# Kernel tuning notes

Hardware: AMD Instinct MI355X
Metric: run time of the kernel (lower is better)

Reference implementation:

```python
import jax, jax.numpy as jnp
import numpy as np

LN_EPS = 1e-5
L2_EPS = 1e-6
TAU = 0.07

def _proj(x, W, b, g, be):
    # Linear + LayerNorm (dropout is identity in eval)
    y = x @ W.T + b
    mu = jnp.mean(y, axis=-1, keepdims=True)
    var = jnp.var(y, axis=-1, keepdims=True)
    return (y - mu) * jax.lax.rsqrt(var + LN_EPS) * g + be

def _l2norm(x):
    return x / (jnp.linalg.norm(x, axis=-1, keepdims=True) + L2_EPS)

def setup_inputs() -> dict:
    key = jax.random.key(0)
    ks = iter(jax.random.split(key, 16))
    B, C, D = 2048, 512, 256
    dims = {"text": 1024, "image": 1024, "audio": 512, "tab": 256}
    inp = {}
    for n, d in dims.items():
        inp[f"f_{n}"] = jax.random.normal(next(ks), (B, d), jnp.float32)
        inp[f"W_{n}"] = jax.random.normal(next(ks), (D, d), jnp.float32) * (1.0 / np.sqrt(d))
        inp[f"b_{n}"] = jnp.zeros((D,), jnp.float32)
        inp[f"g_{n}"] = jnp.ones((D,), jnp.float32)
        inp[f"be_{n}"] = jnp.zeros((D,), jnp.float32)
    inp["U"] = jax.random.normal(next(ks), (C, D), jnp.float32) * (1.0 / np.sqrt(D))
    inp["O"] = jax.random.normal(next(ks), (C, D), jnp.float32) * (1.0 / np.sqrt(D))
    inp["cls_bias"] = jnp.zeros((C,), jnp.float32)
    return inp

def reference(f_text, f_image, f_audio, f_tab,
              W_text, b_text, g_text, be_text,
              W_image, b_image, g_image, be_image,
              W_audio, b_audio, g_audio, be_audio,
              W_tab, b_tab, g_tab, be_tab,
              U, O, cls_bias):
    # Per-modality projection -> Z: [B, M, D]
    Z = jnp.stack([
        _proj(f_text, W_text, b_text, g_text, be_text),
        _proj(f_image, W_image, b_image, g_image, be_image),
        _proj(f_audio, W_audio, b_audio, g_audio, be_audio),
        _proj(f_tab, W_tab, b_tab, g_tab, be_tab),
    ], axis=1)
    Zn = _l2norm(Z)            # [B, M, D]
    Un = _l2norm(U)            # [C, D]
    sim = jnp.einsum('bmd,cd->bmc', Zn, Un) / max(TAU, 1e-6)
    r = jax.nn.softmax(sim, axis=1)                 # softmax over modalities M
    Cmix = jnp.einsum('bmc,bmd->bcd', r, Z)         # [B, C, D]
    logits = jnp.einsum('cd,bcd->bc', O, Cmix) + cls_bias
    OjZi = jnp.einsum('cd,bmd->bmc', O, Z)
    contrib = OjZi * r
    return logits, r, sim, contrib
```

## Files before the change

### kernel.cpp

```cpp
#include <hip/hip_runtime.h>
#include <math.h>

typedef __attribute__((ext_vector_type(8))) short short8;
typedef __attribute__((ext_vector_type(4))) float f32x4;

constexpr int Bn = 2048, Mn = 4, Cn = 512, Dn = 256;
constexpr size_t LOGITS_OFF = 0;
constexpr size_t R_OFF   = (size_t)Bn * Cn;
constexpr size_t SIM_OFF = R_OFF + (size_t)Bn * Mn * Cn;
constexpr size_t CTR_OFF = SIM_OFF + (size_t)Bn * Mn * Cn;
constexpr float INV_TAU = 1.0f / 0.07f;

__device__ __forceinline__ unsigned short f2bf(float f) {
  unsigned u = __float_as_uint(f);
  u += 0x7fffu + ((u >> 16) & 1u);
  return (unsigned short)(u >> 16);
}

__device__ __forceinline__ void gload16(const void* g, void* l) {
  __builtin_amdgcn_global_load_lds(
      (const __attribute__((address_space(1))) void*)g,
      (__attribute__((address_space(3))) void*)l, 16, 0, 0);
}

struct CvtArgs {
  const float* src[6];
  unsigned short* dst[6];
  int n[6];
};

__global__ __launch_bounds__(256) void cvt_kernel(CvtArgs a) {
  int arr = blockIdx.y;
  int idx = (blockIdx.x * 256 + threadIdx.x) * 8;
  if (idx >= a.n[arr]) return;
  const float4* s = (const float4*)(a.src[arr] + idx);
  float4 v0 = s[0], v1 = s[1];
  uint4 p;
  p.x = f2bf(v0.x) | ((unsigned)f2bf(v0.y) << 16);
  p.y = f2bf(v0.z) | ((unsigned)f2bf(v0.w) << 16);
  p.z = f2bf(v1.x) | ((unsigned)f2bf(v1.y) << 16);
  p.w = f2bf(v1.z) | ((unsigned)f2bf(v1.w) << 16);
  *(uint4*)(a.dst[arr] + idx) = p;
}

__global__ __launch_bounds__(256) void invu_kernel(const float* __restrict__ U,
                                                   float* __restrict__ invU) {
  int c = blockIdx.x * 4 + (threadIdx.x >> 6);
  int lane = threadIdx.x & 63;
  float4 v = *(const float4*)&U[(size_t)c * Dn + lane * 4];
  float s = v.x*v.x + v.y*v.y + v.z*v.z + v.w*v.w;
  #pragma unroll
  for (int m = 32; m >= 1; m >>= 1) s += __shfl_xor(s, m, 64);
  if (lane == 0) invU[c] = 1.0f / (sqrtf(s) + 1e-6f);
}

struct ProjArgs {
  const float* f[4];
  const float* b[4];
  const float* g[4];
  const float* be[4];
  const unsigned short* Wb[4];
  int K[4];
};

__global__ __launch_bounds__(128) void proj_kernel(ProjArgs a,
                                                   unsigned short* __restrict__ Zb,
                                                   float* __restrict__ invZ) {
  const int m = blockIdx.y;
  const int row0 = blockIdx.x * 32;
  const int K = a.K[m];
  const float* __restrict__ F = a.f[m];
  const unsigned short* __restrict__ Wm = a.Wb[m];

  __shared__ unsigned short aS[4 * 32 * 8];
  __shared__ unsigned short bS[4 * 256 * 8];
  __shared__ unsigned short zS[32][264];

  const int tid = threadIdx.x;
  const int w = tid >> 6;
  const int l = tid & 63;
  const int rg = l >> 4, c16 = l & 15;

  f32x4 acc[16];
  #pragma unroll
  for (int i = 0; i < 16; i++) acc[i] = (f32x4){0.f, 0.f, 0.f, 0.f};

  const int abase = ((l >> 4) * 32 + w * 16 + c16) * 8;
  const int bbase = ((l >> 4) * 256 + c16) * 8;

  const int akc = tid >> 5;
  const int arow = tid & 31;
  const float* fsrc = F + (size_t)(row0 + arow) * K + akc * 8;

  for (int k0 = 0; k0 < K; k0 += 32) {
    #pragma unroll
    for (int ii = 0; ii < 8; ii++) {
      int i = w + 2 * ii;
      int kc = i >> 2, col = (i & 3) * 64 + l;
      gload16(Wm + (size_t)col * K + k0 + kc * 8, &bS[i * 512]);
    }
    {
      const float4* s = (const float4*)(fsrc + k0);
      float4 v0 = s[0], v1 = s[1];
      uint4 p;
      p.x = f2bf(v0.x) | ((unsigned)f2bf(v0.y) << 16);
      p.y = f2bf(v0.z) | ((unsigned)f2bf(v0.w) << 16);
      p.z = f2bf(v1.x) | ((unsigned)f2bf(v1.y) << 16);
      p.w = f2bf(v1.z) | ((unsigned)f2bf(v1.w) << 16);
      *(uint4*)&aS[tid * 8] = p;
    }
    __syncthreads();
    short8 av = *(const short8*)&aS[abase];
    #pragma unroll
    for (int nf = 0; nf < 16; nf++) {
      short8 bv = *(const short8*)&bS[bbase + nf * 128];
      acc[nf] = __builtin_amdgcn_mfma_f32_16x16x32_bf16(av, bv, acc[nf], 0, 0, 0);
    }
    __syncthreads();
  }

  float bb[16], gg[16], ee[16];
  #pragma unroll
  for (int nf = 0; nf < 16; nf++) {
    bb[nf] = a.b[m][nf * 16 + c16];
    gg[nf] = a.g[m][nf * 16 + c16];
    ee[nf] = a.be[m][nf * 16 + c16];
  }
  float s[4] = {0, 0, 0, 0}, s2[4] = {0, 0, 0, 0};
  #pragma unroll
  for (int nf = 0; nf < 16; nf++) {
    #pragma unroll
    for (int j = 0; j < 4; j++) {
      float y = acc[nf][j] + bb[nf];
      acc[nf][j] = y;
      s[j] += y; s2[j] += y * y;
    }
  }
  #pragma unroll
  for (int msk = 8; msk >= 1; msk >>= 1) {
    #pragma unroll
    for (int j = 0; j < 4; j++) {
      s[j]  += __shfl_xor(s[j],  msk, 64);
      s2[j] += __shfl_xor(s2[j], msk, 64);
    }
  }
  float mu[4], rs[4];
  #pragma unroll
  for (int j = 0; j < 4; j++) {
    mu[j] = s[j] * (1.0f / 256.0f);
    float var = s2[j] * (1.0f / 256.0f) - mu[j] * mu[j];
    rs[j] = rsqrtf(var + 1e-5f);
  }
  float zs[4] = {0, 0, 0, 0};
  #pragma unroll
  for (int nf = 0; nf < 16; nf++) {
    #pragma unroll
    for (int j = 0; j < 4; j++) {
      float z = (acc[nf][j] - mu[j]) * rs[j] * gg[nf] + ee[nf];
      acc[nf][j] = z;
      zs[j] += z * z;
    }
  }
  #pragma unroll
  for (int msk = 8; msk >= 1; msk >>= 1) {
    #pragma unroll
    for (int j = 0; j < 4; j++) zs[j] += __shfl_xor(zs[j], msk, 64);
  }
  float inv[4];
  #pragma unroll
  for (int j = 0; j < 4; j++) inv[j] = 1.0f / (sqrtf(zs[j]) + 1e-6f);

  if (c16 < 4) {
    float v = (c16 == 0) ? inv[0] : (c16 == 1) ? inv[1] : (c16 == 2) ? inv[2] : inv[3];
    int local = w * 16 + rg * 4 + c16;
    invZ[(size_t)(row0 + local) * 4 + m] = v;
  }
  #pragma unroll
  for (int nf = 0; nf < 16; nf++) {
    #pragma unroll
    for (int j = 0; j < 4; j++)
      zS[w * 16 + rg * 4 + j][nf * 16 + c16] = f2bf(acc[nf][j]);
  }
  __syncthreads();
  #pragma unroll
  for (int i = 0; i < 8; i++) {
    int c = tid + i * 128;
    int row = c >> 5, colc = (c & 31) * 8;
    uint4 v = *(const uint4*)&zS[row][colc];
    *(uint4*)(Zb + ((size_t)(row0 + row) * 4 + m) * 256 + colc) = v;
  }
}

__global__ __launch_bounds__(256) void dual_kernel(
    const unsigned short* __restrict__ Zb,
    const unsigned short* __restrict__ Ub,
    const unsigned short* __restrict__ Ob,
    const float* __restrict__ invZ, const float* __restrict__ invU,
    const float* __restrict__ cls_bias, float* __restrict__ out) {
  const int row0 = blockIdx.x * 64;
  const int col0 = blockIdx.y * 128;

  __shared__ unsigned short aS[4 * 64 * 8];
  __shared__ unsigned short uS[4 * 128 * 8];
  __shared__ unsigned short oS[4 * 128 * 8];

  const int tid = threadIdx.x;
  const int w = tid >> 6, l = tid & 63;
  const int wm = w >> 1, wc = w & 1;
  const int rg = l >> 4, c16 = l & 15;

  f32x4 accU[2][4], accO[2][4];
  #pragma unroll
  for (int i = 0; i < 2; i++)
    #pragma unroll
    for (int j = 0; j < 4; j++) {
      accU[i][j] = (f32x4){0.f, 0.f, 0.f, 0.f};
      accO[i][j] = (f32x4){0.f, 0.f, 0.f, 0.f};
    }

  const int abase = ((l >> 4) * 64 + wm * 32 + c16) * 8;
  const int ubase = ((l >> 4) * 128 + wc * 64 + c16) * 8;

  for (int k0 = 0; k0 < 256; k0 += 32) {
    #pragma unroll
    for (int ii = 0; ii < 5; ii++) {
      int i = w + 4 * ii;
      if (i < 4) {
        gload16(Zb + (size_t)(row0 + l) * 256 + k0 + i * 8, &aS[i * 512]);
      } else if (i < 12) {
        int j = i - 4;
        int kc = j >> 1, col = (j & 1) * 64 + l;
        gload16(Ub + (size_t)(col0 + col) * 256 + k0 + kc * 8, &uS[j * 512]);
      } else {
        int j = i - 12;
        int kc = j >> 1, col = (j & 1) * 64 + l;
        gload16(Ob + (size_t)(col0 + col) * 256 + k0 + kc * 8, &oS[j * 512]);
      }
    }
    __syncthreads();
    short8 av0 = *(const short8*)&aS[abase];
    short8 av1 = *(const short8*)&aS[abase + 128];
    #pragma unroll
    for (int nf = 0; nf < 4; nf++) {
      short8 uv = *(const short8*)&uS[ubase + nf * 128];
      accU[0][nf] = __builtin_amdgcn_mfma_f32_16x16x32_bf16(av0, uv, accU[0][nf], 0, 0, 0);
      accU[1][nf] = __builtin_amdgcn_mfma_f32_16x16x32_bf16(av1, uv, accU[1][nf], 0, 0, 0);
      short8 ov = *(const short8*)&oS[ubase + nf * 128];
      accO[0][nf] = __builtin_amdgcn_mfma_f32_16x16x32_bf16(av0, ov, accO[0][nf], 0, 0, 0);
      accO[1][nf] = __builtin_amdgcn_mfma_f32_16x16x32_bf16(av1, ov, accO[1][nf], 0, 0, 0);
    }
    __syncthreads();
  }

  #pragma unroll
  for (int mf = 0; mf < 2; mf++) {
    int bmb = row0 + wm * 32 + mf * 16 + rg * 4;
    f32x4 iz = *(const f32x4*)&invZ[bmb];
    int bidx = bmb >> 2;
    #pragma unroll
    for (int nf = 0; nf < 4; nf++) {
      int col = col0 + wc * 64 + nf * 16 + c16;
      float iu = invU[col] * INV_TAU;
      f32x4 sU = accU[mf][nf], sO = accO[mf][nf];
      float sim0 = sU[0] * iz[0] * iu;
      float sim1 = sU[1] * iz[1] * iu;
      float sim2 = sU[2] * iz[2] * iu;
      float sim3 = sU[3] * iz[3] * iu;
      float mx = fmaxf(fmaxf(sim0, sim1), fmaxf(sim2, sim3));
      float e0 = __expf(sim0 - mx), e1 = __expf(sim1 - mx);
      float e2 = __expf(sim2 - mx), e3 = __expf(sim3 - mx);
      float rinv = 1.0f / (e0 + e1 + e2 + e3);
      float r0 = e0 * rinv, r1 = e1 * rinv, r2 = e2 * rinv, r3 = e3 * rinv;
      float ct0 = sO[0] * r0, ct1 = sO[1] * r1, ct2 = sO[2] * r2, ct3 = sO[3] * r3;
      size_t sb = (size_t)bmb * Cn + col;
      out[SIM_OFF + sb]          = sim0;
      out[SIM_OFF + sb + Cn]     = sim1;
      out[SIM_OFF + sb + 2*Cn]   = sim2;
      out[SIM_OFF + sb + 3*Cn]   = sim3;
      out[R_OFF + sb]            = r0;
      out[R_OFF + sb + Cn]       = r1;
      out[R_OFF + sb + 2*Cn]     = r2;
      out[R_OFF + sb + 3*Cn]     = r3;
      out[CTR_OFF + sb]          = ct0;
      out[CTR_OFF + sb + Cn]     = ct1;
      out[CTR_OFF + sb + 2*Cn]   = ct2;
      out[CTR_OFF + sb + 3*Cn]   = ct3;
      out[LOGITS_OFF + (size_t)bidx * Cn + col] =
          ct0 + ct1 + ct2 + ct3 + cls_bias[col];
    }
  }
}

extern "C" void kernel_launch(void* const* d_in, const int* in_sizes, int n_in,
                              void* d_out, int out_size, void* d_ws, size_t ws_size,
                              hipStream_t stream) {
  const int fi[4] = {0, 5, 10, 15};
  const int Ks[4] = {1024, 1024, 512, 256};

  char* ws = (char*)d_ws;
  unsigned short* Zb  = (unsigned short*)(ws + 0);
  unsigned short* Wb0 = (unsigned short*)(ws + 4194304);
  unsigned short* Wb1 = (unsigned short*)(ws + 4718592);
  unsigned short* Wb2 = (unsigned short*)(ws + 5242880);
  unsigned short* Wb3 = (unsigned short*)(ws + 5505024);
  unsigned short* Ub  = (unsigned short*)(ws + 5636096);
  unsigned short* Ob  = (unsigned short*)(ws + 5898240);
  float* invZ         = (float*)(ws + 6160384);
  float* invU         = (float*)(ws + 6193152);
  unsigned short* Wb[4] = {Wb0, Wb1, Wb2, Wb3};

  ProjArgs pa;
  for (int m = 0; m < 4; m++) {
    pa.f[m]  = (const float*)d_in[fi[m] + 0];
    pa.b[m]  = (const float*)d_in[fi[m] + 2];
    pa.g[m]  = (const float*)d_in[fi[m] + 3];
    pa.be[m] = (const float*)d_in[fi[m] + 4];
    pa.Wb[m] = Wb[m];
    pa.K[m]  = Ks[m];
  }
  const float* U        = (const float*)d_in[20];
  const float* O        = (const float*)d_in[21];
  const float* cls_bias = (const float*)d_in[22];

  CvtArgs ca;
  ca.src[0] = (const float*)d_in[1];   ca.dst[0] = Wb0; ca.n[0] = 262144;
  ca.src[1] = (const float*)d_in[6];   ca.dst[1] = Wb1; ca.n[1] = 262144;
  ca.src[2] = (const float*)d_in[11];  ca.dst[2] = Wb2; ca.n[2] = 131072;
  ca.src[3] = (const float*)d_in[16];  ca.dst[3] = Wb3; ca.n[3] = 65536;
  ca.src[4] = U;                       ca.dst[4] = Ub;  ca.n[4] = 131072;
  ca.src[5] = O;                       ca.dst[5] = Ob;  ca.n[5] = 131072;

  float* out = (float*)d_out;

  cvt_kernel<<<dim3(128, 6), 256, 0, stream>>>(ca);
  invu_kernel<<<128, 256, 0, stream>>>(U, invU);
  proj_kernel<<<dim3(Bn / 32, 4), 128, 0, stream>>>(pa, Zb, invZ);
  dual_kernel<<<dim3((Bn * Mn) / 64, Cn / 128), 256, 0, stream>>>(
      Zb, Ub, Ob, invZ, invU, cls_bias, out);
}
```

Baseline: 192.7 us.

## Drop LDS staging in GEMMs, load MFMA fragments directly from global memory

Both the projection and dual GEMM kernels stop staging tiles in shared memory with barriers. Each wave now loads its MFMA operand fragments straight from global or L2 memory. The projection kernel doubles to 256 threads and splits the 256 output columns across two waves, so the LayerNorm and L2 reductions now combine partial sums through shared memory. The inverse-norm kernel for U is folded into the conversion kernel as an extra grid row, saving one launch. The aim is to remove LDS round-trips and syncthreads stalls, at the cost of more redundant global loads and less data reuse per block.

After: 228.0 us. 18.3% more time.

```diff
diff --git a/kernel.cpp b/kernel.cpp
--- a/kernel.cpp
+++ b/kernel.cpp
@@ -1,4 +1,5 @@
 #include <hip/hip_runtime.h>
+#include <hip/hip_bf16.h>
 #include <math.h>
 
 typedef __attribute__((ext_vector_type(8))) short short8;
@@ -17,10 +18,14 @@
   return (unsigned short)(u >> 16);
 }
 
-__device__ __forceinline__ void gload16(const void* g, void* l) {
-  __builtin_amdgcn_global_load_lds(
-      (const __attribute__((address_space(1))) void*)g,
-      (__attribute__((address_space(3))) void*)l, 16, 0, 0);
+__device__ __forceinline__ short8 cvt8(const float* v) {
+  short8 r;
+  #pragma unroll
+  for (int i = 0; i < 8; i++) {
+    __hip_bfloat16 h = __float2bfloat16(v[i]);
+    r[i] = (short)*reinterpret_cast<unsigned short*>(&h);
+  }
+  return r;
 }
 
 struct CvtArgs {
@@ -29,8 +34,20 @@
   int n[6];
 };
 
-__global__ __launch_bounds__(256) void cvt_kernel(CvtArgs a) {
+__global__ __launch_bounds__(256) void cvt_kernel(CvtArgs a,
+                                                  const float* __restrict__ U,
+                                                  float* __restrict__ invU) {
   int arr = blockIdx.y;
+  if (arr == 6) {
+    int c = blockIdx.x * 4 + (threadIdx.x >> 6);
+    int lane = threadIdx.x & 63;
+    float4 v = *(const float4*)&U[(size_t)c * Dn + lane * 4];
+    float s = v.x*v.x + v.y*v.y + v.z*v.z + v.w*v.w;
+    #pragma unroll
+    for (int m = 32; m >= 1; m >>= 1) s += __shfl_xor(s, m, 64);
+    if (lane == 0) invU[c] = 1.0f / (sqrtf(s) + 1e-6f);
+    return;
+  }
   int idx = (blockIdx.x * 256 + threadIdx.x) * 8;
   if (idx >= a.n[arr]) return;
   const float4* s = (const float4*)(a.src[arr] + idx);
@@ -43,17 +60,6 @@
   *(uint4*)(a.dst[arr] + idx) = p;
 }
 
-__global__ __launch_bounds__(256) void invu_kernel(const float* __restrict__ U,
-                                                   float* __restrict__ invU) {
-  int c = blockIdx.x * 4 + (threadIdx.x >> 6);
-  int lane = threadIdx.x & 63;
-  float4 v = *(const float4*)&U[(size_t)c * Dn + lane * 4];
-  float s = v.x*v.x + v.y*v.y + v.z*v.z + v.w*v.w;
-  #pragma unroll
-  for (int m = 32; m >= 1; m >>= 1) s += __shfl_xor(s, m, 64);
-  if (lane == 0) invU[c] = 1.0f / (sqrtf(s) + 1e-6f);
-}
-
 struct ProjArgs {
   const float* f[4];
   const float* b[4];
@@ -63,131 +69,126 @@
   int K[4];
 };
 
-__global__ __launch_bounds__(128) void proj_kernel(ProjArgs a,
+__global__ __launch_bounds__(256) void proj_kernel(ProjArgs a,
                                                    unsigned short* __restrict__ Zb,
                                                    float* __restrict__ invZ) {
   const int m = blockIdx.y;
-  const int row0 = blockIdx.x * 32;
   const int K = a.K[m];
   const float* __restrict__ F = a.f[m];
   const unsigned short* __restrict__ Wm = a.Wb[m];
 
-  __shared__ unsigned short aS[4 * 32 * 8];
-  __shared__ unsigned short bS[4 * 256 * 8];
+  const int tid = threadIdx.x;
+  const int w = tid >> 6, l = tid & 63;
+  const int wm = w >> 1, wc = w & 1;
+  const int rg = l >> 4, c16 = l & 15;
+  const int row0 = blockIdx.x * 32 + wm * 16;
+
+  __shared__ float pS[2][16][2][2];
+  __shared__ float qS[2][16][2][2];
   __shared__ unsigned short zS[32][264];
 
-  const int tid = threadIdx.x;
-  const int w = tid >> 6;
-  const int l = tid & 63;
-  const int rg = l >> 4, c16 = l & 15;
-
-  f32x4 acc[16];
-  #pragma unroll
-  for (int i = 0; i < 16; i++) acc[i] = (f32x4){0.f, 0.f, 0.f, 0.f};
-
-  const int abase = ((l >> 4) * 32 + w * 16 + c16) * 8;
-  const int bbase = ((l >> 4) * 256 + c16) * 8;
-
-  const int akc = tid >> 5;
-  const int arow = tid & 31;
-  const float* fsrc = F + (size_t)(row0 + arow) * K + akc * 8;
-
+  f32x4 acc[8];
+  #pragma unroll
+  for (int i = 0; i < 8; i++) acc[i] = (f32x4){0.f, 0.f, 0.f, 0.f};
+
+  const float* aptr = F + (size_t)(row0 + c16) * K + rg * 8;
+  const unsigned short* bptr = Wm + (size_t)(wc * 128 + c16) * K + rg * 8;
+
+  #pragma unroll 2
   for (int k0 = 0; k0 < K; k0 += 32) {
-    #pragma unroll
-    for (int ii = 0; ii < 8; ii++) {
-      int i = w + 2 * ii;
-      int kc = i >> 2, col = (i & 3) * 64 + l;
-      gload16(Wm + (size_t)col * K + k0 + kc * 8, &bS[i * 512]);
-    }
-    {
-      const float4* s = (const float4*)(fsrc + k0);
-      float4 v0 = s[0], v1 = s[1];
-      uint4 p;
-      p.x = f2bf(v0.x) | ((unsigned)f2bf(v0.y) << 16);
-      p.y = f2bf(v0.z) | ((unsigned)f2bf(v0.w) << 16);
-      p.z = f2bf(v1.x) | ((unsigned)f2bf(v1.y) << 16);
-      p.w = f2bf(v1.z) | ((unsigned)f2bf(v1.w) << 16);
-      *(uint4*)&aS[tid * 8] = p;
-    }
-    __syncthreads();
-    short8 av = *(const short8*)&aS[abase];
-    #pragma unroll
-    for (int nf = 0; nf < 16; nf++) {
-      short8 bv = *(const short8*)&bS[bbase + nf * 128];
-      acc[nf] = __builtin_amdgcn_mfma_f32_16x16x32_bf16(av, bv, acc[nf], 0, 0, 0);
-    }
-    __syncthreads();
-  }
-
-  float bb[16], gg[16], ee[16];
-  #pragma unroll
-  for (int nf = 0; nf < 16; nf++) {
-    bb[nf] = a.b[m][nf * 16 + c16];
-    gg[nf] = a.g[m][nf * 16 + c16];
-    ee[nf] = a.be[m][nf * 16 + c16];
-  }
-  float s[4] = {0, 0, 0, 0}, s2[4] = {0, 0, 0, 0};
-  #pragma unroll
-  for (int nf = 0; nf < 16; nf++) {
+    float av[8];
+    *(float4*)&av[0] = *(const float4*)(aptr + k0);
+    *(float4*)&av[4] = *(const float4*)(aptr + k0 + 4);
+    short8 af = cvt8(av);
+    #pragma unroll
+    for (int nf = 0; nf < 8; nf++) {
+      short8 bv = *(const short8*)(bptr + (size_t)nf * 16 * K + k0);
+      acc[nf] = __builtin_amdgcn_mfma_f32_16x16x32_bf16(af, bv, acc[nf], 0, 0, 0);
+    }
+  }
+
+  float bb[8], gg[8], ee[8];
+  #pragma unroll
+  for (int nf = 0; nf < 8; nf++) {
+    int col = wc * 128 + nf * 16 + c16;
+    bb[nf] = a.b[m][col];
+    gg[nf] = a.g[m][col];
+    ee[nf] = a.be[m][col];
+  }
+  float s[4] = {0,0,0,0}, s2[4] = {0,0,0,0};
+  #pragma unroll
+  for (int nf = 0; nf < 8; nf++)
     #pragma unroll
     for (int j = 0; j < 4; j++) {
       float y = acc[nf][j] + bb[nf];
       acc[nf][j] = y;
       s[j] += y; s2[j] += y * y;
     }
-  }
-  #pragma unroll
-  for (int msk = 8; msk >= 1; msk >>= 1) {
+  #pragma unroll
+  for (int msk = 8; msk >= 1; msk >>= 1)
     #pragma unroll
     for (int j = 0; j < 4; j++) {
       s[j]  += __shfl_xor(s[j],  msk, 64);
       s2[j] += __shfl_xor(s2[j], msk, 64);
     }
-  }
+  if (c16 == 0)
+    #pragma unroll
+    for (int j = 0; j < 4; j++) {
+      pS[wm][rg*4+j][wc][0] = s[j];
+      pS[wm][rg*4+j][wc][1] = s2[j];
+    }
+  __syncthreads();
   float mu[4], rs[4];
   #pragma unroll
   for (int j = 0; j < 4; j++) {
-    mu[j] = s[j] * (1.0f / 256.0f);
-    float var = s2[j] * (1.0f / 256.0f) - mu[j] * mu[j];
+    float st  = pS[wm][rg*4+j][0][0] + pS[wm][rg*4+j][1][0];
+    float s2t = pS[wm][rg*4+j][0][1] + pS[wm][rg*4+j][1][1];
+    mu[j] = st * (1.0f/256.0f);
+    float var = s2t * (1.0f/256.0f) - mu[j]*mu[j];
     rs[j] = rsqrtf(var + 1e-5f);
   }
-  float zs[4] = {0, 0, 0, 0};
-  #pragma unroll
-  for (int nf = 0; nf < 16; nf++) {
+  float zs[4] = {0,0,0,0};
+  #pragma unroll
+  for (int nf = 0; nf < 8; nf++)
     #pragma unroll
     for (int j = 0; j < 4; j++) {
       float z = (acc[nf][j] - mu[j]) * rs[j] * gg[nf] + ee[nf];
       acc[nf][j] = z;
       zs[j] += z * z;
     }
-  }
-  #pragma unroll
-  for (int msk = 8; msk >= 1; msk >>= 1) {
+  #pragma unroll
+  for (int msk = 8; msk >= 1; msk >>= 1)
     #pragma unroll
     for (int j = 0; j < 4; j++) zs[j] += __shfl_xor(zs[j], msk, 64);
-  }
+  if (c16 == 0)
+    #pragma unroll
+    for (int j = 0; j < 4; j++) {
+      qS[wm][rg*4+j][wc][0] = zs[j];
+    }
+  __syncthreads();
   float inv[4];
   #pragma unroll
-  for (int j = 0; j < 4; j++) inv[j] = 1.0f / (sqrtf(zs[j]) + 1e-6f);
-
-  if (c16 < 4) {
-    float v = (c16 == 0) ? inv[0] : (c16 == 1) ? inv[1] : (c16 == 2) ? inv[2] : inv[3];
-    int local = w * 16 + rg * 4 + c16;
-    invZ[(size_t)(row0 + local) * 4 + m] = v;
-  }
-  #pragma unroll
-  for (int nf = 0; nf < 16; nf++) {
+  for (int j = 0; j < 4; j++) {
+    float zt = qS[wm][rg*4+j][0][0] + qS[wm][rg*4+j][1][0];
+    inv[j] = 1.0f / (sqrtf(zt) + 1e-6f);
+  }
+  if (c16 == 0 && wc == 0)
     #pragma unroll
     for (int j = 0; j < 4; j++)
-      zS[w * 16 + rg * 4 + j][nf * 16 + c16] = f2bf(acc[nf][j]);
-  }
+      invZ[(size_t)(row0 + rg*4 + j) * 4 + m] = inv[j];
+
+  #pragma unroll
+  for (int nf = 0; nf < 8; nf++)
+    #pragma unroll
+    for (int j = 0; j < 4; j++)
+      zS[wm*16 + rg*4 + j][wc*128 + nf*16 + c16] = f2bf(acc[nf][j]);
   __syncthreads();
   #pragma unroll
-  for (int i = 0; i < 8; i++) {
-    int c = tid + i * 128;
+  for (int i = 0; i < 4; i++) {
+    int c = tid + i * 256;
     int row = c >> 5, colc = (c & 31) * 8;
     uint4 v = *(const uint4*)&zS[row][colc];
-    *(uint4*)(Zb + ((size_t)(row0 + row) * 4 + m) * 256 + colc) = v;
+    *(uint4*)(Zb + ((size_t)(blockIdx.x * 32 + row) * 4 + m) * 256 + colc) = v;
   }
 }
 
@@ -197,97 +198,68 @@
     const unsigned short* __restrict__ Ob,
     const float* __restrict__ invZ, const float* __restrict__ invU,
     const float* __restrict__ cls_bias, float* __restrict__ out) {
-  const int row0 = blockIdx.x * 64;
-  const int col0 = blockIdx.y * 128;
-
-  __shared__ unsigned short aS[4 * 64 * 8];
-  __shared__ unsigned short uS[4 * 128 * 8];
-  __shared__ unsigned short oS[4 * 128 * 8];
-
   const int tid = threadIdx.x;
   const int w = tid >> 6, l = tid & 63;
-  const int wm = w >> 1, wc = w & 1;
   const int rg = l >> 4, c16 = l & 15;
-
-  f32x4 accU[2][4], accO[2][4];
-  #pragma unroll
-  for (int i = 0; i < 2; i++)
-    #pragma unroll
-    for (int j = 0; j < 4; j++) {
-      accU[i][j] = (f32x4){0.f, 0.f, 0.f, 0.f};
-      accO[i][j] = (f32x4){0.f, 0.f, 0.f, 0.f};
-    }
-
-  const int abase = ((l >> 4) * 64 + wm * 32 + c16) * 8;
-  const int ubase = ((l >> 4) * 128 + wc * 64 + c16) * 8;
-
+  const int row0 = blockIdx.x * 64 + w * 16;
+  const int col0 = blockIdx.y * 128;
+
+  f32x4 accU[8], accO[8];
+  #pragma unroll
+  for (int i = 0; i < 8; i++) {
+    accU[i] = (f32x4){0.f, 0.f, 0.f, 0.f};
+    accO[i] = (f32x4){0.f, 0.f, 0.f, 0.f};
+  }
+
+  const unsigned short* aptr = Zb + (size_t)(row0 + c16) * 256 + rg * 8;
+  const unsigned short* uptr = Ub + (size_t)(col0 + c16) * 256 + rg * 8;
+  const unsigned short* optr = Ob + (size_t)(col0 + c16) * 256 + rg * 8;
+
+  #pragma unroll 2
   for (int k0 = 0; k0 < 256; k0 += 32) {
-    #pragma unroll
-    for (int ii = 0; ii < 5; ii++) {
-      int i = w + 4 * ii;
-      if (i < 4) {
-        gload16(Zb + (size_t)(row0 + l) * 256 + k0 + i * 8, &aS[i * 512]);
-      } else if (i < 12) {
-        int j = i - 4;
-        int kc = j >> 1, col = (j & 1) * 64 + l;
-        gload16(Ub + (size_t)(col0 + col) * 256 + k0 + kc * 8, &uS[j * 512]);
-      } else {
-        int j = i - 12;
-        int kc = j >> 1, col = (j & 1) * 64 + l;
-        gload16(Ob + (size_t)(col0 + col) * 256 + k0 + kc * 8, &oS[j * 512]);
-      }
-    }
-    __syncthreads();
-    short8 av0 = *(const short8*)&aS[abase];
-    short8 av1 = *(const short8*)&aS[abase + 128];
-    #pragma unroll
-    for (int nf = 0; nf < 4; nf++) {
-      short8 uv = *(const short8*)&uS[ubase + nf * 128];
-      accU[0][nf] = __builtin_amdgcn_mfma_f32_16x16x32_bf16(av0, uv, accU[0][nf], 0, 0, 0);
-      accU[1][nf] = __builtin_amdgcn_mfma_f32_16x16x32_bf16(av1, uv, accU[1][nf], 0, 0, 0);
-      short8 ov = *(const short8*)&oS[ubase + nf * 128];
-      accO[0][nf] = __builtin_amdgcn_mfma_f32_16x16x32_bf16(av0, ov, accO[0][nf], 0, 0, 0);
-      accO[1][nf] = __builtin_amdgcn_mfma_f32_16x16x32_bf16(av1, ov, accO[1][nf], 0, 0, 0);
-    }
-    __syncthreads();
-  }
-
-  #pragma unroll
-  for (int mf = 0; mf < 2; mf++) {
-    int bmb = row0 + wm * 32 + mf * 16 + rg * 4;
-    f32x4 iz = *(const f32x4*)&invZ[bmb];
-    int bidx = bmb >> 2;
-    #pragma unroll
-    for (int nf = 0; nf < 4; nf++) {
-      int col = col0 + wc * 64 + nf * 16 + c16;
-      float iu = invU[col] * INV_TAU;
-      f32x4 sU = accU[mf][nf], sO = accO[mf][nf];
-      float sim0 = sU[0] * iz[0] * iu;
-      float sim1 = sU[1] * iz[1] * iu;
-      float sim2 = sU[2] * iz[2] * iu;
-      float sim3 = sU[3] * iz[3] * iu;
-      float mx = fmaxf(fmaxf(sim0, sim1), fmaxf(sim2, sim3));
-      float e0 = __expf(sim0 - mx), e1 = __expf(sim1 - mx);
-      float e2 = __expf(sim2 - mx), e3 = __expf(sim3 - mx);
-      float rinv = 1.0f / (e0 + e1 + e2 + e3);
-      float r0 = e0 * rinv, r1 = e1 * rinv, r2 = e2 * rinv, r3 = e3 * rinv;
-      float ct0 = sO[0] * r0, ct1 = sO[1] * r1, ct2 = sO[2] * r2, ct3 = sO[3] * r3;
-      size_t sb = (size_t)bmb * Cn + col;
-      out[SIM_OFF + sb]          = sim0;
-      out[SIM_OFF + sb + Cn]     = sim1;
-      out[SIM_OFF + sb + 2*Cn]   = sim2;
-      out[SIM_OFF + sb + 3*Cn]   = sim3;
-      out[R_OFF + sb]            = r0;
-      out[R_OFF + sb + Cn]       = r1;
-      out[R_OFF + sb + 2*Cn]     = r2;
-      out[R_OFF + sb + 3*Cn]     = r3;
-      out[CTR_OFF + sb]          = ct0;
-      out[CTR_OFF + sb + Cn]     = ct1;
-      out[CTR_OFF + sb + 2*Cn]   = ct2;
-      out[CTR_OFF + sb + 3*Cn]   = ct3;
-      out[LOGITS_OFF + (size_t)bidx * Cn + col] =
-          ct0 + ct1 + ct2 + ct3 + cls_bias[col];
-    }
+    short8 av = *(const short8*)(aptr + k0);
+    #pragma unroll
+    for (int nf = 0; nf < 8; nf++) {
+      short8 uv = *(const short8*)(uptr + (size_t)nf * 16 * 256 + k0);
+      accU[nf] = __builtin_amdgcn_mfma_f32_16x16x32_bf16(av, uv, accU[nf], 0, 0, 0);
+      short8 ov = *(const short8*)(optr + (size_t)nf * 16 * 256 + k0);
+      accO[nf] = __builtin_amdgcn_mfma_f32_16x16x32_bf16(av, ov, accO[nf], 0, 0, 0);
+    }
+  }
+
+  const int bmb = row0 + rg * 4;
+  const f32x4 iz = *(const f32x4*)&invZ[bmb];
+  const int bidx = bmb >> 2;
+  #pragma unroll
+  for (int nf = 0; nf < 8; nf++) {
+    int col = col0 + nf * 16 + c16;
+    float iu = invU[col] * INV_TAU;
+    f32x4 sU = accU[nf], sO = accO[nf];
+    float sim0 = sU[0] * iz[0] * iu;
+    float sim1 = sU[1] * iz[1] * iu;
+    float sim2 = sU[2] * iz[2] * iu;
+    float sim3 = sU[3] * iz[3] * iu;
+    float mx = fmaxf(fmaxf(sim0, sim1), fmaxf(sim2, sim3));
+    float e0 = __expf(sim0 - mx), e1 = __expf(sim1 - mx);
+    float e2 = __expf(sim2 - mx), e3 = __expf(sim3 - mx);
+    float rinv = 1.0f / (e0 + e1 + e2 + e3);
+    float r0 = e0 * rinv, r1 = e1 * rinv, r2 = e2 * rinv, r3 = e3 * rinv;
+    float ct0 = sO[0] * r0, ct1 = sO[1] * r1, ct2 = sO[2] * r2, ct3 = sO[3] * r3;
+    size_t sb = (size_t)bmb * Cn + col;
+    out[SIM_OFF + sb]        = sim0;
+    out[SIM_OFF + sb + Cn]   = sim1;
+    out[SIM_OFF + sb + 2*Cn] = sim2;
+    out[SIM_OFF + sb + 3*Cn] = sim3;
+    out[R_OFF + sb]          = r0;
+    out[R_OFF + sb + Cn]     = r1;
+    out[R_OFF + sb + 2*Cn]   = r2;
+    out[R_OFF + sb + 3*Cn]   = r3;
+    out[CTR_OFF + sb]        = ct0;
+    out[CTR_OFF + sb + Cn]   = ct1;
+    out[CTR_OFF + sb + 2*Cn] = ct2;
+    out[CTR_OFF + sb + 3*Cn] = ct3;
+    out[LOGITS_OFF + (size_t)bidx * Cn + col] =
+        ct0 + ct1 + ct2 + ct3 + cls_bias[col];
   }
 }
 
@@ -332,9 +304,8 @@
 
   float* out = (float*)d_out;
 
-  cvt_kernel<<<dim3(128, 6), 256, 0, stream>>>(ca);
-  invu_kernel<<<128, 256, 0, stream>>>(U, invU);
-  proj_kernel<<<dim3(Bn / 32, 4), 128, 0, stream>>>(pa, Zb, invZ);
+  cvt_kernel<<<dim3(128, 7), 256, 0, stream>>>(ca, U, invU);
+  proj_kernel<<<dim3(Bn / 32, 4), 256, 0, stream>>>(pa, Zb, invZ);
   dual_kernel<<<dim3((Bn * Mn) / 64, Cn / 128), 256, 0, stream>>>(
       Zb, Ub, Ob, invZ, invU, cls_bias, out);
 }
```
